# Performance work log

Hardware: AMD Instinct MI355X
Metric: run time of the kernel (lower is better)

Reference implementation:

```python
import jax, jax.numpy as jnp
import numpy as np
import math

B, S, D_MODEL = 4, 2048, 1024
H, D_QK, D_V = 16, 64, 64


def setup_inputs() -> dict:
    key = jax.random.key(0)
    ks = jax.random.split(key, 12)
    s = 0.02
    return {
        "input_q": jax.random.normal(ks[0], (B, S, D_MODEL), jnp.float32),
        "input_k": jax.random.normal(ks[1], (B, S, D_MODEL), jnp.float32),
        "input_v": jax.random.normal(ks[2], (B, S, D_MODEL), jnp.float32),
        # per-head projection weights stacked over heads: [H, out, d_model] (torch Linear layout)
        "WQw": jax.random.normal(ks[3], (H, D_QK, D_MODEL), jnp.float32) * s,
        "WQb": jax.random.normal(ks[4], (H, D_QK), jnp.float32) * s,
        "WKw": jax.random.normal(ks[5], (H, D_QK, D_MODEL), jnp.float32) * s,
        "WKb": jax.random.normal(ks[6], (H, D_QK), jnp.float32) * s,
        "WVw": jax.random.normal(ks[7], (H, D_V, D_MODEL), jnp.float32) * s,
        "WVb": jax.random.normal(ks[8], (H, D_V), jnp.float32) * s,
        # output projection: Linear(H*D_V, D_MODEL)
        "Ww": jax.random.normal(ks[9], (D_MODEL, H * D_V), jnp.float32) * s,
        "Wb": jax.random.normal(ks[10], (D_MODEL,), jnp.float32) * s,
    }


def _mha(input_q, input_k, input_v, WQw, WQb, WKw, WKb, WVw, WVb, Ww, Wb):
    # per-head projections: [B,H,S,d]
    Q = jnp.einsum("bsd,hed->bhse", input_q, WQw) + WQb[None, :, None, :]
    K = jnp.einsum("bsd,hed->bhse", input_k, WKw) + WKb[None, :, None, :]
    V = jnp.einsum("bsd,hvd->bhsv", input_v, WVw) + WVb[None, :, None, :]
    scores = jnp.einsum("bhse,bhte->bhst", Q, K)  # [B,H,S,S]
    # causal mask added BEFORE division by sqrt(d_model), as in original
    causal = jnp.triu(jnp.full((S, S), -jnp.inf, scores.dtype), k=1)
    scores = (scores + causal) / math.sqrt(D_MODEL)  # NOTE: d_model, not d_qk
    attn = jax.nn.softmax(scores, axis=-1)
    ctx = jnp.einsum("bhst,bhtv->bhsv", attn, V)  # [B,H,S,D_V]
    concat = ctx.transpose(0, 2, 1, 3).reshape(B, S, H * D_V)  # head-order concat
    return concat @ Ww.T + Wb


def reference(input_q, input_k, input_v, WQw, WQb, WKw, WKb, WVw, WVb, Ww, Wb):
    return _mha(input_q, input_k, input_v, WQw, WQb, WKw, WKb, WVw, WVb, Ww, Wb)
```

## Files before the change

kernel.cpp:

```cpp
#include <hip/hip_runtime.h>
#include <hip/hip_bf16.h>

typedef __attribute__((ext_vector_type(8))) short bf16x8;
typedef __attribute__((ext_vector_type(4))) short bf16x4;
typedef __attribute__((ext_vector_type(4))) float f32x4;
typedef __attribute__((ext_vector_type(16))) float f32x16;
typedef __attribute__((ext_vector_type(4))) unsigned uint4v;

#define MFMA16(a, b, c) __builtin_amdgcn_mfma_f32_16x16x32_bf16(a, b, c, 0, 0, 0)
#define MFMA32(a, b, c) __builtin_amdgcn_mfma_f32_32x32x16_bf16(a, b, c, 0, 0, 0)

__device__ __forceinline__ unsigned short f2bfn(float f) {
#if defined(__gfx950__)
  __bf16 h = (__bf16)f;
  return __builtin_bit_cast(unsigned short, h);
#else
  union { float f; unsigned u; } x; x.f = f;
  unsigned r = x.u + 0x7fffu + ((x.u >> 16) & 1u);
  return (unsigned short)(r >> 16);
#endif
}

__device__ __forceinline__ void plswap(unsigned& a, unsigned& b) {
  auto r = __builtin_amdgcn_permlane32_swap(a, b, false, false);
  a = r[0];
  b = r[1];
}

__device__ __forceinline__ unsigned cvtpk(float lo, float hi) {
  unsigned w;
  asm("v_cvt_pk_bf16_f32 %0, %1, %2" : "=v"(w) : "v"(lo), "v"(hi));
  return w;
}

__device__ __forceinline__ void cvt_body(const float* __restrict__ s,
                                         unsigned short* __restrict__ d, int n8) {
  int i = blockIdx.x * blockDim.x + threadIdx.x;
  int st = gridDim.x * blockDim.x;
  for (; i < n8; i += st) {
    const float4* sp = reinterpret_cast<const float4*>(s) + 2 * (size_t)i;
    float4 a = sp[0], b = sp[1];
    uint4v o;
    o[0] = cvtpk(a.x, a.y); o[1] = cvtpk(a.z, a.w);
    o[2] = cvtpk(b.x, b.y); o[3] = cvtpk(b.z, b.w);
    reinterpret_cast<uint4v*>(d)[i] = o;
  }
}

__global__ void cvt1_kernel(const float* __restrict__ s, unsigned short* __restrict__ d, int n8) {
  cvt_body(s, d, n8);
}

__global__ void cvt_w_kernel(const float* s0, const float* s1, const float* s2, const float* s3,
                             unsigned short* d0, unsigned short* d1, unsigned short* d2,
                             unsigned short* d3, int n8) {
  const float* s; unsigned short* d;
  switch (blockIdx.y) {
    case 0: s = s0; d = d0; break;
    case 1: s = s1; d = d1; break;
    case 2: s = s2; d = d2; break;
    default: s = s3; d = d3; break;
  }
  cvt_body(s, d, n8);
}

template <int MODE>
__global__ __launch_bounds__(256) void gemm_kernel(
    const unsigned short* __restrict__ Av, const unsigned short* __restrict__ Bv,
    const float* __restrict__ bias, void* __restrict__ outv,
    int M, int N, int K) {
  constexpr int BM = 128, BN = 128, BK = 64;
  __shared__ __align__(16) unsigned short As[2][BM * BK];
  __shared__ __align__(16) unsigned short Bs[2][BN * BK];
  const int tid = threadIdx.x;
  const int lane = tid & 63, wave = tid >> 6;
  const int wr = wave >> 1, wc = wave & 1;
  const int m0 = blockIdx.y * BM, n0 = blockIdx.x * BN;
  const int rb = lane & 15, g = lane >> 4;
  const int swz = ((lane & 7) ^ ((lane >> 3) & 7)) * 8;
  f32x4 acc[4][4] = {};

  const unsigned short* Ab = Av + (size_t)m0 * K;
  const unsigned short* Bb = Bv + (size_t)n0 * K;

  auto stage = [&](int buf, int k0) {
#pragma unroll
    for (int i = 0; i < 4; ++i) {
      const int c = wave * 256 + i * 64 + lane;
      const int r = c >> 3;
      __builtin_amdgcn_global_load_lds(
          (const __attribute__((address_space(1))) unsigned int*)(Ab + (size_t)r * K + k0 + swz),
          (__attribute__((address_space(3))) unsigned int*)&As[buf][c * 8], 16, 0, 0);
      __builtin_amdgcn_global_load_lds(
          (const __attribute__((address_space(1))) unsigned int*)(Bb + (size_t)r * K + k0 + swz),
          (__attribute__((address_space(3))) unsigned int*)&Bs[buf][c * 8], 16, 0, 0);
    }
  };

  const int nt = K / BK;
  stage(0, 0);
  int cur = 0;
  for (int t = 0; t < nt; ++t) {
    __syncthreads();
    if (t + 1 < nt) stage(cur ^ 1, (t + 1) * BK);
    const unsigned short* A_ = As[cur];
    const unsigned short* B_ = Bs[cur];
#pragma unroll
    for (int kc = 0; kc < 2; ++kc) {
      bf16x8 af[4], bfr[4];
#pragma unroll
      for (int mi = 0; mi < 4; ++mi)
        af[mi] = *reinterpret_cast<const bf16x8*>(
            &A_[(wr * 64 + mi * 16 + rb) * 64 + (((kc * 4 + g) ^ (rb & 7)) * 8)]);
#pragma unroll
      for (int ni = 0; ni < 4; ++ni)
        bfr[ni] = *reinterpret_cast<const bf16x8*>(
            &B_[(wc * 64 + ni * 16 + rb) * 64 + (((kc * 4 + g) ^ (rb & 7)) * 8)]);
#pragma unroll
      for (int mi = 0; mi < 4; ++mi)
#pragma unroll
        for (int ni = 0; ni < 4; ++ni)
          acc[mi][ni] = MFMA16(af[mi], bfr[ni], acc[mi][ni]);
    }
    cur ^= 1;
  }

#pragma unroll
  for (int mi = 0; mi < 4; ++mi) {
#pragma unroll
    for (int ni = 0; ni < 4; ++ni) {
      int col = n0 + wc * 64 + ni * 16 + rb;
      if constexpr (MODE != 2) {
        float bv = bias[col];
#pragma unroll
        for (int j = 0; j < 4; ++j) {
          int row = m0 + wr * 64 + mi * 16 + g * 4 + j;
          float v = acc[mi][ni][j] + bv;
          if constexpr (MODE == 0) {
            int b = row >> 11, s = row & 2047;
            int h = col >> 6, e = col & 63;
            ((unsigned short*)outv)[((size_t)(b * 16 + h) * 2048 + s) * 64 + e] = f2bfn(v);
          } else {
            ((float*)outv)[(size_t)row * N + col] = v;
          }
        }
      } else {
        int bb = col >> 11, s = col & 2047;
#pragma unroll
        for (int j = 0; j < 4; ++j) {
          int row = m0 + wr * 64 + mi * 16 + g * 4 + j;
          float v = acc[mi][ni][j] + bias[row];
          int h = row >> 6, e = row & 63;
          ((unsigned short*)outv)[((size_t)(bb * 16 + h) * 64 + e) * 2048 + s] = f2bfn(v);
        }
      }
    }
  }
}

__global__ __launch_bounds__(256) void attn5_kernel(
    const unsigned short* __restrict__ Qp, const unsigned short* __restrict__ Kp,
    const unsigned short* __restrict__ Vtp, unsigned short* __restrict__ ctx) {
  constexpr int S = 2048;
  __shared__ __align__(16) unsigned short Ks[2][64 * 64];
  __shared__ __align__(16) unsigned short Vs[2][64 * 64];
  const int bx = blockIdx.x;
  const int bh = bx & 63;
  const int qti = 15 - (bx >> 6);
  const int q0 = qti * 128;
  const int tid = threadIdx.x, wave = tid >> 6, lane = tid & 63;
  const int l31 = lane & 31, hb = lane >> 5, hb4 = hb * 4;
  const int x7 = l31 & 7;
  const int qw = q0 + wave * 32;
  const unsigned short* Qb = Qp + (size_t)bh * S * 64;
  const unsigned short* Kb = Kp + (size_t)bh * S * 64;
  const unsigned short* Vb = Vtp + (size_t)bh * 64 * S;

  bf16x8 qg[4];
#pragma unroll
  for (int kc = 0; kc < 4; ++kc)
    qg[kc] = *reinterpret_cast<const bf16x8*>(
        Qb + (size_t)(qw + l31) * 64 + 16 * kc + 8 * hb);

  float lsum = 0.f;
  f32x16 o[2] = {};
  const float sc = 0.03125f * 1.4426950408889634f;
  const float SH = -2.0f;
  const int sswz = ((lane & 7) ^ (lane >> 3)) * 8;
  const int nt = qti * 2 + 2;

  auto stage = [&](int buf, int kv0) {
#pragma unroll
    for (int i = 0; i < 2; ++i) {
      const int ci = (wave * 2 + i) * 64 + lane;
      const int r = (wave * 2 + i) * 8 + (lane >> 3);
      __builtin_amdgcn_global_load_lds(
          (const __attribute__((address_space(1))) unsigned int*)(Kb + (size_t)(kv0 + r) * 64 + sswz),
          (__attribute__((address_space(3))) unsigned int*)&Ks[buf][ci * 8], 16, 0, 0);
      __builtin_amdgcn_global_load_lds(
          (const __attribute__((address_space(1))) unsigned int*)(Vb + (size_t)r * S + kv0 + sswz),
          (__attribute__((address_space(3))) unsigned int*)&Vs[buf][ci * 8], 16, 0, 0);
    }
  };

  stage(0, 0);

  for (int it = 0; it < nt; ++it) {
    __syncthreads();
    if (it + 1 < nt) stage((it + 1) & 1, 64 * (it + 1));
    const int kv0 = 64 * it;
    if (kv0 <= qw + 31) {
      const unsigned short* K_ = Ks[it & 1];
      const unsigned short* V_ = Vs[it & 1];
      f32x16 sacc[2] = {};
      __builtin_amdgcn_s_setprio(1);
#pragma unroll
      for (int kc = 0; kc < 4; ++kc) {
        bf16x8 kf0 = *reinterpret_cast<const bf16x8*>(
            &K_[l31 * 64 + ((2 * kc + hb) ^ x7) * 8]);
        bf16x8 kf1 = *reinterpret_cast<const bf16x8*>(
            &K_[(32 + l31) * 64 + ((2 * kc + hb) ^ x7) * 8]);
        sacc[0] = MFMA32(kf0, qg[kc], sacc[0]);
        sacc[1] = MFMA32(kf1, qg[kc], sacc[1]);
      }
      __builtin_amdgcn_s_setprio(0);
      if (kv0 + 63 > qw) {
        const int qrel = qw + l31 - kv0;
#pragma unroll
        for (int mi = 0; mi < 2; ++mi)
#pragma unroll
          for (int r = 0; r < 16; ++r) {
            int koff = 32 * mi + (r & 3) + 8 * (r >> 2) + hb4;
            if (koff > qrel) sacc[mi][r] = -1e30f;
          }
      }
      float p0[16], p1[16];
#pragma unroll
      for (int r = 0; r < 16; ++r)
        p0[r] = __builtin_amdgcn_exp2f(fmaf(sacc[0][r], sc, SH));
#pragma unroll
      for (int r = 0; r < 16; ++r)
        p1[r] = __builtin_amdgcn_exp2f(fmaf(sacc[1][r], sc, SH));
      unsigned pw[2][8];
#pragma unroll
      for (int i = 0; i < 8; ++i) pw[0][i] = cvtpk(p0[2 * i], p0[2 * i + 1]);
#pragma unroll
      for (int i = 0; i < 8; ++i) pw[1][i] = cvtpk(p1[2 * i], p1[2 * i + 1]);
      float a[16];
#pragma unroll
      for (int r = 0; r < 16; ++r) a[r] = p0[r] + p1[r];
#pragma unroll
      for (int s = 8; s > 0; s >>= 1)
#pragma unroll
        for (int r = 0; r < s; ++r) a[r] += a[r + s];
      lsum += a[0];
#pragma unroll
      for (int mi = 0; mi < 2; ++mi) {
        plswap(pw[mi][0], pw[mi][2]);
        plswap(pw[mi][1], pw[mi][3]);
        plswap(pw[mi][4], pw[mi][6]);
        plswap(pw[mi][5], pw[mi][7]);
      }
      __builtin_amdgcn_s_setprio(1);
#pragma unroll
      for (int c = 0; c < 4; ++c) {
        union { unsigned u[4]; bf16x8 v; } pu;
        pu.u[0] = pw[c >> 1][(c & 1) * 4 + 0];
        pu.u[1] = pw[c >> 1][(c & 1) * 4 + 1];
        pu.u[2] = pw[c >> 1][(c & 1) * 4 + 2];
        pu.u[3] = pw[c >> 1][(c & 1) * 4 + 3];
#pragma unroll
        for (int db = 0; db < 2; ++db) {
          bf16x8 vf = *reinterpret_cast<const bf16x8*>(
              &V_[(32 * db + l31) * 64 + ((2 * c + hb) ^ x7) * 8]);
          o[db] = MFMA32(vf, pu.v, o[db]);
        }
      }
      __builtin_amdgcn_s_setprio(0);
    }
  }

  const float tot = lsum + __shfl_xor(lsum, 32, 64);
  const float inv = 1.0f / tot;
  const int b = bh >> 4, h = bh & 15;
  const int q = qw + l31;
  unsigned short* cp = ctx + ((size_t)(b * 2048 + q) * 1024) + h * 64;
#pragma unroll
  for (int db = 0; db < 2; ++db)
#pragma unroll
    for (int i = 0; i < 8; ++i) {
      unsigned w = cvtpk(o[db][2 * i] * inv, o[db][2 * i + 1] * inv);
      int d = 32 * db + ((2 * i) & 3) + 8 * (i >> 1) + hb4;
      *reinterpret_cast<unsigned*>(cp + d) = w;
    }
}

extern "C" void kernel_launch(void* const* d_in, const int* in_sizes, int n_in,
                              void* d_out, int out_size, void* d_ws, size_t ws_size,
                              hipStream_t stream) {
  const float* in_q = (const float*)d_in[0];
  const float* in_k = (const float*)d_in[1];
  const float* in_v = (const float*)d_in[2];
  const float* WQw = (const float*)d_in[3];
  const float* WQb = (const float*)d_in[4];
  const float* WKw = (const float*)d_in[5];
  const float* WKb = (const float*)d_in[6];
  const float* WVw = (const float*)d_in[7];
  const float* WVb = (const float*)d_in[8];
  const float* Ww  = (const float*)d_in[9];
  const float* Wb  = (const float*)d_in[10];
  float* out = (float*)d_out;

  constexpr size_t PROJ = (size_t)4 * 16 * 2048 * 64;
  constexpr size_t WSZ = (size_t)1024 * 1024;
  unsigned short* wsp = (unsigned short*)d_ws;
  unsigned short* Qp   = wsp;
  unsigned short* Kp   = wsp + PROJ;
  unsigned short* Vt   = wsp + 2 * PROJ;
  unsigned short* in16 = wsp + 3 * PROJ;
  unsigned short* ctx  = in16;
  unsigned short* wq16 = wsp + 4 * PROJ;
  unsigned short* wk16 = wq16 + WSZ;
  unsigned short* wv16 = wk16 + WSZ;
  unsigned short* ww16 = wv16 + WSZ;

  cvt_w_kernel<<<dim3(256, 4), 256, 0, stream>>>(WQw, WKw, WVw, Ww,
                                                 wq16, wk16, wv16, ww16, (int)(WSZ / 8));
  cvt1_kernel<<<2048, 256, 0, stream>>>(in_q, in16, (int)(PROJ / 8));
  gemm_kernel<0><<<dim3(8, 64), 256, 0, stream>>>(in16, wq16, WQb, Qp, 8192, 1024, 1024);
  cvt1_kernel<<<2048, 256, 0, stream>>>(in_k, in16, (int)(PROJ / 8));
  gemm_kernel<0><<<dim3(8, 64), 256, 0, stream>>>(in16, wk16, WKb, Kp, 8192, 1024, 1024);
  cvt1_kernel<<<2048, 256, 0, stream>>>(in_v, in16, (int)(PROJ / 8));
  gemm_kernel<2><<<dim3(64, 8), 256, 0, stream>>>(wv16, in16, WVb, Vt, 1024, 8192, 1024);

  attn5_kernel<<<1024, 256, 0, stream>>>(Qp, Kp, Vt, ctx);

  gemm_kernel<1><<<dim3(8, 64), 256, 0, stream>>>(ctx, ww16, Wb, out, 8192, 1024, 1024);
}
```

Before: 192.1 us.

## Fuse fp32-to-bf16 input conversion into projection GEMM loads; reorder attention tiles

The three standalone activation conversion kernels are removed. The projection GEMMs now load fp32 activations straight into registers, convert them to bf16 and write them into swizzled LDS after the MFMA loop, which saves a full read and write of the bf16 intermediate per input. The attention kernel also maps block index to query tile through a fixed permutation that interleaves long and short causal tiles, aiming for better load balance. In exchange the GEMM uses more registers, and the fp32 stores to LDS are no longer asynchronous, which may reduce overlap.

```diff
diff --git a/kernel.cpp b/kernel.cpp
--- a/kernel.cpp
+++ b/kernel.cpp
@@ -47,10 +47,6 @@
   }
 }
 
-__global__ void cvt1_kernel(const float* __restrict__ s, unsigned short* __restrict__ d, int n8) {
-  cvt_body(s, d, n8);
-}
-
 __global__ void cvt_w_kernel(const float* s0, const float* s1, const float* s2, const float* s3,
                              unsigned short* d0, unsigned short* d1, unsigned short* d2,
                              unsigned short* d3, int n8) {
@@ -66,9 +62,11 @@
 
 template <int MODE>
 __global__ __launch_bounds__(256) void gemm_kernel(
-    const unsigned short* __restrict__ Av, const unsigned short* __restrict__ Bv,
+    const void* __restrict__ Av, const void* __restrict__ Bv,
     const float* __restrict__ bias, void* __restrict__ outv,
     int M, int N, int K) {
+  constexpr bool AF32 = (MODE == 0);
+  constexpr bool BF32 = (MODE == 2);
   constexpr int BM = 128, BN = 128, BK = 64;
   __shared__ __align__(16) unsigned short As[2][BM * BK];
   __shared__ __align__(16) unsigned short Bs[2][BN * BK];
@@ -80,29 +78,80 @@
   const int swz = ((lane & 7) ^ ((lane >> 3) & 7)) * 8;
   f32x4 acc[4][4] = {};
 
-  const unsigned short* Ab = Av + (size_t)m0 * K;
-  const unsigned short* Bb = Bv + (size_t)n0 * K;
-
-  auto stage = [&](int buf, int k0) {
+  const unsigned short* Ab16 = (const unsigned short*)Av + (size_t)m0 * K;
+  const unsigned short* Bb16 = (const unsigned short*)Bv + (size_t)n0 * K;
+  const float* Ab32 = (const float*)Av + (size_t)m0 * K;
+  const float* Bb32 = (const float*)Bv + (size_t)n0 * K;
+
+  auto gload = [&](const unsigned short* base, unsigned short* dst, int k0) {
 #pragma unroll
     for (int i = 0; i < 4; ++i) {
       const int c = wave * 256 + i * 64 + lane;
       const int r = c >> 3;
       __builtin_amdgcn_global_load_lds(
-          (const __attribute__((address_space(1))) unsigned int*)(Ab + (size_t)r * K + k0 + swz),
-          (__attribute__((address_space(3))) unsigned int*)&As[buf][c * 8], 16, 0, 0);
-      __builtin_amdgcn_global_load_lds(
-          (const __attribute__((address_space(1))) unsigned int*)(Bb + (size_t)r * K + k0 + swz),
-          (__attribute__((address_space(3))) unsigned int*)&Bs[buf][c * 8], 16, 0, 0);
+          (const __attribute__((address_space(1))) unsigned int*)(base + (size_t)r * K + k0 + swz),
+          (__attribute__((address_space(3))) unsigned int*)&dst[c * 8], 16, 0, 0);
     }
   };
+  auto f32issue = [&](const float* base, int k0, float4* v) {
+#pragma unroll
+    for (int j = 0; j < 4; ++j) {
+      const int d = tid + 256 * j;
+      const int r = d >> 3, ch = d & 7;
+      const float* p = base + (size_t)r * K + k0 + ch * 8;
+      v[2 * j] = *reinterpret_cast<const float4*>(p);
+      v[2 * j + 1] = *reinterpret_cast<const float4*>(p + 4);
+    }
+  };
+  auto f32write = [&](unsigned short* T, const float4* v) {
+#pragma unroll
+    for (int j = 0; j < 4; ++j) {
+      const int d = tid + 256 * j;
+      const int r = d >> 3, ch = d & 7;
+      uint4v o;
+      o[0] = cvtpk(v[2 * j].x, v[2 * j].y);
+      o[1] = cvtpk(v[2 * j].z, v[2 * j].w);
+      o[2] = cvtpk(v[2 * j + 1].x, v[2 * j + 1].y);
+      o[3] = cvtpk(v[2 * j + 1].z, v[2 * j + 1].w);
+      *reinterpret_cast<uint4v*>(&T[r * 64 + ((ch ^ (r & 7)) * 8)]) = o;
+    }
+  };
 
   const int nt = K / BK;
-  stage(0, 0);
+  {
+    float4 fv[8];
+    if constexpr (AF32) {
+      f32issue(Ab32, 0, fv);
+      gload(Bb16, Bs[0], 0);
+      f32write(As[0], fv);
+    } else if constexpr (BF32) {
+      f32issue(Bb32, 0, fv);
+      gload(Ab16, As[0], 0);
+      f32write(Bs[0], fv);
+    } else {
+      gload(Ab16, As[0], 0);
+      gload(Bb16, Bs[0], 0);
+    }
+  }
+
   int cur = 0;
   for (int t = 0; t < nt; ++t) {
     __syncthreads();
-    if (t + 1 < nt) stage(cur ^ 1, (t + 1) * BK);
+    const bool more = (t + 1 < nt);
+    const int k1 = (t + 1) * BK;
+    float4 nv[8];
+    if (more) {
+      if constexpr (AF32) {
+        gload(Bb16, Bs[cur ^ 1], k1);
+        f32issue(Ab32, k1, nv);
+      } else if constexpr (BF32) {
+        gload(Ab16, As[cur ^ 1], k1);
+        f32issue(Bb32, k1, nv);
+      } else {
+        gload(Ab16, As[cur ^ 1], k1);
+        gload(Bb16, Bs[cur ^ 1], k1);
+      }
+    }
     const unsigned short* A_ = As[cur];
     const unsigned short* B_ = Bs[cur];
 #pragma unroll
@@ -121,6 +170,10 @@
 #pragma unroll
         for (int ni = 0; ni < 4; ++ni)
           acc[mi][ni] = MFMA16(af[mi], bfr[ni], acc[mi][ni]);
+    }
+    if (more) {
+      if constexpr (AF32) f32write(As[cur ^ 1], nv);
+      if constexpr (BF32) f32write(Bs[cur ^ 1], nv);
     }
     cur ^= 1;
   }
@@ -164,9 +217,10 @@
   constexpr int S = 2048;
   __shared__ __align__(16) unsigned short Ks[2][64 * 64];
   __shared__ __align__(16) unsigned short Vs[2][64 * 64];
+  const int qtimap16[16] = {15, 13, 11, 9, 0, 2, 4, 6, 14, 12, 10, 8, 1, 3, 5, 7};
   const int bx = blockIdx.x;
   const int bh = bx & 63;
-  const int qti = 15 - (bx >> 6);
+  const int qti = qtimap16[bx >> 6];
   const int q0 = qti * 128;
   const int tid = threadIdx.x, wave = tid >> 6, lane = tid & 63;
   const int l31 = lane & 31, hb = lane >> 5, hb4 = hb * 4;
@@ -317,8 +371,7 @@
   unsigned short* Qp   = wsp;
   unsigned short* Kp   = wsp + PROJ;
   unsigned short* Vt   = wsp + 2 * PROJ;
-  unsigned short* in16 = wsp + 3 * PROJ;
-  unsigned short* ctx  = in16;
+  unsigned short* ctx  = wsp + 3 * PROJ;
   unsigned short* wq16 = wsp + 4 * PROJ;
   unsigned short* wk16 = wq16 + WSZ;
   unsigned short* wv16 = wk16 + WSZ;
@@ -326,12 +379,9 @@
 
   cvt_w_kernel<<<dim3(256, 4), 256, 0, stream>>>(WQw, WKw, WVw, Ww,
                                                  wq16, wk16, wv16, ww16, (int)(WSZ / 8));
-  cvt1_kernel<<<2048, 256, 0, stream>>>(in_q, in16, (int)(PROJ / 8));
-  gemm_kernel<0><<<dim3(8, 64), 256, 0, stream>>>(in16, wq16, WQb, Qp, 8192, 1024, 1024);
-  cvt1_kernel<<<2048, 256, 0, stream>>>(in_k, in16, (int)(PROJ / 8));
-  gemm_kernel<0><<<dim3(8, 64), 256, 0, stream>>>(in16, wk16, WKb, Kp, 8192, 1024, 1024);
-  cvt1_kernel<<<2048, 256, 0, stream>>>(in_v, in16, (int)(PROJ / 8));
-  gemm_kernel<2><<<dim3(64, 8), 256, 0, stream>>>(wv16, in16, WVb, Vt, 1024, 8192, 1024);
+  gemm_kernel<0><<<dim3(8, 64), 256, 0, stream>>>(in_q, wq16, WQb, Qp, 8192, 1024, 1024);
+  gemm_kernel<0><<<dim3(8, 64), 256, 0, stream>>>(in_k, wk16, WKb, Kp, 8192, 1024, 1024);
+  gemm_kernel<2><<<dim3(64, 8), 256, 0, stream>>>(wv16, in_v, WVb, Vt, 1024, 8192, 1024);
 
   attn5_kernel<<<1024, 256, 0, stream>>>(Qp, Kp, Vt, ctx);
 
```

Result: slower. 212.0 us (+10.3%).
